# Performance work log

Measured on AMD Instinct MI355X. Metric: run time of the kernel, lower is better.

The kernel has to match this reference:

```python
import jax, jax.numpy as jnp
import numpy as np

PI = np.pi
TAU = 1.0        # self.tau
TAU_V = 10.0     # self.tau_v
TAU_CONN = 10.0  # self.tau_conn
TAU_E = 1000.0   # self.tau_e
GW = PI / 4      # gauss_width
GH = 3.0         # gauss_height
LR = 10000.0     # hebbian lr
SPIKE_NUM = 4    # keep_top_n count
NORM_FAC_HD = 1.0


def period_bound(d):
    # wrap to (-pi, pi]
    return (d + PI) % (2.0 * PI) - PI


def dist(d):
    d = period_bound(d)
    return jnp.where(d > PI, d - 2.0 * PI, d)


def setup_inputs() -> dict:
    key = jax.random.key(0)
    ks = jax.random.split(key, 8)
    P, num, L = 20000, 256, 30
    return {
        "conn_bearing": jnp.abs(jax.random.normal(ks[0], (P, num, L), jnp.float32) * 0.1),
        "r": jax.random.uniform(ks[1], (num,), jnp.float32) * 0.1,
        "u": jax.random.uniform(ks[2], (num,), jnp.float32) * 0.5,
        "v": jax.random.uniform(ks[3], (num,), jnp.float32) * 0.1,
        "r_hpc": jax.random.uniform(ks[4], (P,), jnp.float32),
        "r_bearing": jax.random.uniform(ks[5], (L,), jnp.float32),
        "pos_estimate": jnp.zeros((1,), jnp.float32),
        "angular_velocity": jnp.float32(0.3),
        "HD": jnp.float32(0.5),
        "sen2HD_stre": jnp.float32(1.0),
        "shared_t": jnp.arange(2, dtype=jnp.float32) * 0.1,  # [0, dt]
        "noise_hd": jax.random.normal(ks[6], (num,), jnp.float32) * 0.01,
        "noise_bearing": jax.random.normal(ks[7], (L,), jnp.float32) * 0.01,
        "dt": 0.1,
    }


def reference(conn_bearing, r, u, v, r_hpc, r_bearing, pos_estimate,
              angular_velocity, HD, sen2HD_stre, shared_t,
              noise_hd, noise_bearing, dt):
    # One HdOVCModel.update step with get_HD=0, noise_stre=0.0, train=2.
    P, num, L = conn_bearing.shape
    k = 0.8 / num * 20.0
    J0 = 1.0 / num * 20.0
    m = 0.84 * TAU / TAU_V
    x = jnp.linspace(-PI, PI, num + 1)[:-1]  # ring preferred directions

    # ring connectivity kernel + its FFT (precomputed in __init__)
    d0 = dist(jnp.abs(x[0] - x))
    conn = J0 * jnp.exp(-0.5 * jnp.square(d0 / GW)) / (2.0 * PI * GW ** 2)
    conn_fft = jnp.fft.fft(conn)

    # get_center(r, x) == angle(sum(exp(1j x) * r)), done in reals
    center = jnp.arctan2(jnp.sum(jnp.sin(x) * r), jnp.sum(jnp.cos(x) * r))

    # self_motion_integrate (noise_stre = 0)
    pos_e = pos_estimate + (period_bound(center - pos_estimate) / TAU_E + angular_velocity) * dt
    pos_est = period_bound(pos_e)  # [1]
    motion_input = GH * jnp.exp(-0.25 * jnp.square(dist(x - pos_est) / GW))  # [num]
    Iext = motion_input  # get_HD == 0 branch (input_HD(HD) unused)

    # bearing input via hippocampal place weighting
    r_place = r_hpc[:P]
    index = jnp.argmax(r_place)
    norm_r = jnp.where(r_place == 0, 0.0, r_place / jnp.sum(r_place))
    # fused matmul [P,num,L]@[L] then weighted sum over P
    input_bearing = jnp.einsum('pnl,l,p->n', conn_bearing, r_bearing, norm_r)

    # recurrent ring input via circular convolution (FFT)
    Irec = jnp.real(jnp.fft.ifft(jnp.fft.fft(r) * conn_fft))
    input_total = Iext + Irec + input_bearing * sen2HD_stre

    # derivative() is linear with CONSTANT coupling terms (uses self.u/self.v,
    # not the integrated state), so odeint has an exact closed form:
    # du/dt = (-u + Cu)/tau, dv/dt = (-v + Cv)/tau_v
    t = shared_t[1] - shared_t[0]
    Cu = input_total - v
    Cv = m * u
    u_sol = Cu + (u - Cu) * jnp.exp(-t / TAU)
    v_sol = Cv + (v - Cv) * jnp.exp(-t / TAU_V)
    u_new = jnp.maximum(u_sol, 0.0)
    v_new = v_sol
    r1 = jnp.square(u_new)
    r_new = r1 / (1.0 + k * jnp.sum(r1))

    # conn_update (train == 2): gather row -> top-k Hebb -> normalize -> scatter
    cb_row = conn_bearing[index]                         # [num, L]
    r_hd = r_new * (1.0 + jnp.abs(noise_hd))
    topv = jax.lax.top_k(r_hd, SPIKE_NUM)[0]
    r_learn = jnp.where(r_hd >= topv[-1], r_hd, 0.0)     # keep_top_n
    rb = r_bearing + jnp.abs(noise_bearing)
    corr = jnp.outer(r_learn, rb)                        # [num, L]
    d_b = LR * corr * cb_row / TAU_CONN * dt
    cb = cb_row + d_b
    cb = NORM_FAC_HD * cb / jnp.sum(cb, axis=1, keepdims=True)  # normalize_rows
    conn_bearing_new = conn_bearing.at[index].set(cb)

    return r_new, u_new, v_new, conn_bearing_new
```

## Files before the change

kernel.cpp:

```cpp
#include <hip/hip_runtime.h>

#define PI_F 3.14159265358979323846f
#define TWO_PI_F 6.28318530717958647692f

#define TAU_F 1.0f
#define TAU_V_F 10.0f
#define TAU_CONN_F 10.0f
#define TAU_E_F 1000.0f
#define GW_F (PI_F / 4.0f)
#define GH_F 3.0f
#define LR_F 10000.0f

#define NUMN 256
#define LB 30
#define SLAB (NUMN * LB)
#define SLAB4 (SLAB / 4)

__device__ __forceinline__ float pbf(float d) {
  float m = fmodf(d + PI_F, TWO_PI_F);
  if (m < 0.f) m += TWO_PI_F;
  return m - PI_F;
}

__global__ __launch_bounds__(256) void k_reduce_hpc(const float* __restrict__ r_hpc,
                                                    int P, float* __restrict__ ws) {
  __shared__ float ssum[256];
  __shared__ float smax[256];
  __shared__ int simax[256];
  int t = threadIdx.x;
  float s = 0.f;
  float bm = -1e30f;
  int bi = 0x7fffffff;
  for (int i = t; i < P; i += 256) {
    float v = r_hpc[i];
    s += v;
    if (v > bm) { bm = v; bi = i; }
  }
  ssum[t] = s; smax[t] = bm; simax[t] = bi;
  __syncthreads();
  for (int off = 128; off > 0; off >>= 1) {
    if (t < off) {
      ssum[t] += ssum[t + off];
      float vo = smax[t + off]; int io = simax[t + off];
      if (vo > smax[t] || (vo == smax[t] && io < simax[t])) { smax[t] = vo; simax[t] = io; }
    }
    __syncthreads();
  }
  if (t == 0) {
    ws[0] = ssum[0];
    ((int*)ws)[1] = simax[0];
  }
}

__global__ __launch_bounds__(256) void k_main(const float* __restrict__ cb,
                                              const float* __restrict__ r_hpc,
                                              const float* __restrict__ r_bearing,
                                              const float* __restrict__ ws_scal,
                                              float* __restrict__ partial,
                                              float* __restrict__ out_cb,
                                              int P, int chunk) {
  __shared__ __align__(16) float slab[SLAB];
  __shared__ float rbs[32];
  int t = threadIdx.x;
  int blk = blockIdx.x;
  if (t < LB) rbs[t] = r_bearing[t];
  float S = ws_scal[0];
  float acc = 0.f;
  int p0 = blk * chunk;
  int p1 = p0 + chunk; if (p1 > P) p1 = P;
  for (int p = p0; p < p1; ++p) {
    const float4* in4 = (const float4*)(cb + (size_t)p * SLAB);
    float4* o4 = (float4*)(out_cb + (size_t)p * SLAB);
    float4* s4 = (float4*)slab;
    for (int i = t; i < SLAB4; i += 256) {
      float4 v = in4[i];
      s4[i] = v;
      o4[i] = v;
    }
    __syncthreads();
    float rp = r_hpc[p];
    float w = (rp == 0.f) ? 0.f : rp / S;
    const float* row = slab + t * LB;
    float dot = 0.f;
#pragma unroll
    for (int l = 0; l < LB; ++l) dot += row[l] * rbs[l];
    acc += w * dot;
    __syncthreads();
  }
  partial[(size_t)blk * NUMN + t] = acc;
}

__global__ __launch_bounds__(256) void k_reduce_partial(const float* __restrict__ partial,
                                                        float* __restrict__ p2, int nb) {
  int t = threadIdx.x;
  int j = blockIdx.x;
  float s = 0.f;
  for (int b = j; b < nb; b += 64) s += partial[(size_t)b * NUMN + t];
  p2[(size_t)j * NUMN + t] = s;
}

__device__ __forceinline__ float block_reduce_sum(float val, float* red, int t) {
  red[t] = val;
  __syncthreads();
  for (int off = 128; off > 0; off >>= 1) {
    if (t < off) red[t] += red[t + off];
    __syncthreads();
  }
  float r0 = red[0];
  __syncthreads();
  return r0;
}

__global__ __launch_bounds__(256) void k_finish(
    const float* __restrict__ cb,
    const float* __restrict__ r, const float* __restrict__ u, const float* __restrict__ v,
    const float* __restrict__ noise_hd,
    const float* __restrict__ r_bearing, const float* __restrict__ noise_bearing,
    const float* __restrict__ pos_estimate, const float* __restrict__ angular_velocity,
    const float* __restrict__ sen2HD_stre, const float* __restrict__ shared_t,
    const float* __restrict__ dtp,
    const float* __restrict__ ws_scal, const float* __restrict__ p2,
    float* __restrict__ out) {
  __shared__ float red[256];
  __shared__ float rL[256], connL[256], rhdL[256];
  __shared__ float rbL[32];
  __shared__ float bc[8];
  int t = threadIdx.x;
  int index = ((const int*)ws_scal)[1];

  float ib = 0.f;
  for (int j = 0; j < 64; ++j) ib += p2[(size_t)j * NUMN + t];

  float x = -PI_F + (float)t * (TWO_PI_F / 256.f);
  float rt = r[t];
  rL[t] = rt;

  float ssin = block_reduce_sum(sinf(x) * rt, red, t);
  float scos = block_reduce_sum(cosf(x) * rt, red, t);

  if (t == 0) {
    float center = atan2f(ssin, scos);
    float pe = pos_estimate[0];
    float dtv = dtp[0];
    float pos_e = pe + (pbf(center - pe) / TAU_E_F + angular_velocity[0]) * dtv;
    bc[0] = pbf(pos_e);
  }
  __syncthreads();
  float pos_est = bc[0];

  {
    float J0 = 20.f / 256.f;
    float dmin = fminf((float)t, 256.f - (float)t) * (TWO_PI_F / 256.f);
    float q = dmin / GW_F;
    connL[t] = J0 * expf(-0.5f * q * q) / (TWO_PI_F * GW_F * GW_F);
  }
  __syncthreads();

  float Irec = 0.f;
  for (int m2 = 0; m2 < 256; ++m2) Irec += rL[m2] * connL[(t - m2) & 255];

  float dd = pbf(x - pos_est);
  float qq = dd / GW_F;
  float Iext = GH_F * expf(-0.25f * qq * qq);

  float input_total = Iext + Irec + ib * sen2HD_stre[0];
  float tstep = shared_t[1] - shared_t[0];
  float e1 = expf(-tstep / TAU_F);
  float e2 = expf(-tstep / TAU_V_F);
  float mcoef = 0.84f * TAU_F / TAU_V_F;

  float ut = u[t], vt = v[t];
  float Cu = input_total - vt;
  float Cv = mcoef * ut;
  float u_sol = Cu + (ut - Cu) * e1;
  float v_sol = Cv + (vt - Cv) * e2;
  float u_new = fmaxf(u_sol, 0.f);
  float r1 = u_new * u_new;
  float s1 = block_reduce_sum(r1, red, t);
  float kcoef = 0.8f / 256.f * 20.f;
  float r_new = r1 / (1.f + kcoef * s1);

  out[t] = r_new;
  out[256 + t] = u_new;
  out[512 + t] = v_sol;

  rhdL[t] = r_new * (1.f + fabsf(noise_hd[t]));
  if (t < LB) rbL[t] = r_bearing[t] + fabsf(noise_bearing[t]);
  __syncthreads();

  if (t == 0) {
    int e0 = -1, e1i = -1, e2i = -1, e3 = -1;
    float thr = 0.f;
    for (int pass = 0; pass < 4; ++pass) {
      float bm = -1e30f; int bi = -1;
      for (int i2 = 0; i2 < 256; ++i2) {
        if (i2 == e0 || i2 == e1i || i2 == e2i || i2 == e3) continue;
        float vv = rhdL[i2];
        if (vv > bm) { bm = vv; bi = i2; }
      }
      if (pass == 0) e0 = bi; else if (pass == 1) e1i = bi; else if (pass == 2) e2i = bi; else e3 = bi;
      thr = bm;
    }
    bc[1] = thr;
  }
  __syncthreads();
  float thr = bc[1];
  float r_learn = (rhdL[t] >= thr) ? rhdL[t] : 0.f;

  float dtv = dtp[0];
  float fac = (LR_F / TAU_CONN_F) * dtv;
  const float* rowp = cb + ((size_t)index * NUMN + t) * LB;
  float vals[LB];
  float s = 0.f;
#pragma unroll
  for (int l = 0; l < LB; ++l) {
    float vv = rowp[l] * (1.f + fac * r_learn * rbL[l]);
    vals[l] = vv;
    s += vv;
  }
  float inv = 1.f / s;
  float* orow = out + 768 + ((size_t)index * NUMN + t) * LB;
#pragma unroll
  for (int l = 0; l < LB; ++l) orow[l] = vals[l] * inv;
}

extern "C" void kernel_launch(void* const* d_in, const int* in_sizes, int n_in,
                              void* d_out, int out_size, void* d_ws, size_t ws_size,
                              hipStream_t stream) {
  const float* conn_bearing = (const float*)d_in[0];
  const float* r            = (const float*)d_in[1];
  const float* u            = (const float*)d_in[2];
  const float* v            = (const float*)d_in[3];
  const float* r_hpc        = (const float*)d_in[4];
  const float* r_bearing    = (const float*)d_in[5];
  const float* pos_estimate = (const float*)d_in[6];
  const float* angular_vel  = (const float*)d_in[7];
  const float* sen2HD       = (const float*)d_in[9];
  const float* shared_t     = (const float*)d_in[10];
  const float* noise_hd     = (const float*)d_in[11];
  const float* noise_bear   = (const float*)d_in[12];
  const float* dtp          = (const float*)d_in[13];

  int P = in_sizes[4];

  float* out = (float*)d_out;
  float* ws = (float*)d_ws;

  const int OFF_P2 = 16;
  const int OFF_PART = OFF_P2 + 64 * NUMN;

  int nb = 2000;
  {
    size_t avail = ws_size / 4;
    if (avail < (size_t)OFF_PART + NUMN) {
      nb = 1;
    } else {
      size_t maxnb = (avail - OFF_PART) / NUMN;
      if ((size_t)nb > maxnb) nb = (int)maxnb;
      if (nb < 1) nb = 1;
    }
  }
  int chunk = (P + nb - 1) / nb;

  k_reduce_hpc<<<1, 256, 0, stream>>>(r_hpc, P, ws);
  k_main<<<nb, 256, 0, stream>>>(conn_bearing, r_hpc, r_bearing, ws,
                                 ws + OFF_PART, out + 768, P, chunk);
  k_reduce_partial<<<64, 256, 0, stream>>>(ws + OFF_PART, ws + OFF_P2, nb);
  k_finish<<<1, 256, 0, stream>>>(conn_bearing, r, u, v, noise_hd, r_bearing, noise_bear,
                                  pos_estimate, angular_vel, sen2HD, shared_t, dtp,
                                  ws, ws + OFF_P2, out);
}
```

Before: 368.0 us.

## Drop LDS staging in main pass; process two slabs per iteration with nontemporal copy

Removes the shared-memory slab staging and per-slab barriers in the main streaming kernel. Each iteration now copies two slabs to the output with nontemporal stores, and each half of the block computes dot products for one slab by reading global rows directly, relying on cache hits. r_bearing is held in registers, launch bounds request 3 blocks per CU, and the block count rises from 2000 to 2500. The cost is re-reading slab data from global/cache for the dot products and higher register pressure.

```diff
diff --git a/kernel.cpp b/kernel.cpp
--- a/kernel.cpp
+++ b/kernel.cpp
@@ -15,6 +15,9 @@
 #define LB 30
 #define SLAB (NUMN * LB)
 #define SLAB4 (SLAB / 4)
+
+typedef float fx4 __attribute__((ext_vector_type(4)));
+typedef float fx2 __attribute__((ext_vector_type(2)));
 
 __device__ __forceinline__ float pbf(float d) {
   float m = fmodf(d + PI_F, TWO_PI_F);
@@ -52,42 +55,80 @@
   }
 }
 
-__global__ __launch_bounds__(256) void k_main(const float* __restrict__ cb,
-                                              const float* __restrict__ r_hpc,
-                                              const float* __restrict__ r_bearing,
-                                              const float* __restrict__ ws_scal,
-                                              float* __restrict__ partial,
-                                              float* __restrict__ out_cb,
-                                              int P, int chunk) {
-  __shared__ __align__(16) float slab[SLAB];
-  __shared__ float rbs[32];
+__global__ __launch_bounds__(256, 3) void k_main(const float* __restrict__ cb,
+                                                 const float* __restrict__ r_hpc,
+                                                 const float* __restrict__ r_bearing,
+                                                 const float* __restrict__ ws_scal,
+                                                 float* __restrict__ partial,
+                                                 float* __restrict__ out_cb,
+                                                 int P, int chunk) {
+  __shared__ float pacc[2][NUMN];
   int t = threadIdx.x;
   int blk = blockIdx.x;
-  if (t < LB) rbs[t] = r_bearing[t];
   float S = ws_scal[0];
-  float acc = 0.f;
+
+  float rbv[LB];
+#pragma unroll
+  for (int l = 0; l < LB; ++l) rbv[l] = r_bearing[l];
+
+  int which = t >> 7;
+  int pair  = t & 127;
+  int n0 = pair * 2;
+
+  float acc0 = 0.f, acc1 = 0.f, accT = 0.f;
+
   int p0 = blk * chunk;
   int p1 = p0 + chunk; if (p1 > P) p1 = P;
-  for (int p = p0; p < p1; ++p) {
-    const float4* in4 = (const float4*)(cb + (size_t)p * SLAB);
-    float4* o4 = (float4*)(out_cb + (size_t)p * SLAB);
-    float4* s4 = (float4*)slab;
+  int p = p0;
+  for (; p + 1 < p1; p += 2) {
+    const fx4* __restrict__ in4 = (const fx4*)(cb + (size_t)p * SLAB);
+    fx4* __restrict__ o4 = (fx4*)(out_cb + (size_t)p * SLAB);
+#pragma unroll
+    for (int k = 0; k < 15; ++k) {
+      int i = t + k * 256;
+      fx4 tmp = in4[i];
+      __builtin_nontemporal_store(tmp, o4 + i);
+    }
+    int pp = p + which;
+    float rp = r_hpc[pp];
+    float w = (rp == 0.f) ? 0.f : rp / S;
+    const fx4* __restrict__ row4 = (const fx4*)(cb + (size_t)pp * SLAB + n0 * LB);
+    float d0 = 0.f, d1 = 0.f;
+#pragma unroll
+    for (int k = 0; k < 15; ++k) {
+      fx4 vv = row4[k];
+      int e = 4 * k;
+      if (e + 0 < LB) d0 += vv.x * rbv[e + 0]; else d1 += vv.x * rbv[e + 0 - LB];
+      if (e + 1 < LB) d0 += vv.y * rbv[e + 1]; else d1 += vv.y * rbv[e + 1 - LB];
+      if (e + 2 < LB) d0 += vv.z * rbv[e + 2]; else d1 += vv.z * rbv[e + 2 - LB];
+      if (e + 3 < LB) d0 += vv.w * rbv[e + 3]; else d1 += vv.w * rbv[e + 3 - LB];
+    }
+    acc0 += w * d0;
+    acc1 += w * d1;
+  }
+  if (p < p1) {
+    const fx4* __restrict__ in4 = (const fx4*)(cb + (size_t)p * SLAB);
+    fx4* __restrict__ o4 = (fx4*)(out_cb + (size_t)p * SLAB);
     for (int i = t; i < SLAB4; i += 256) {
-      float4 v = in4[i];
-      s4[i] = v;
-      o4[i] = v;
-    }
-    __syncthreads();
+      fx4 tmp = in4[i];
+      __builtin_nontemporal_store(tmp, o4 + i);
+    }
     float rp = r_hpc[p];
     float w = (rp == 0.f) ? 0.f : rp / S;
-    const float* row = slab + t * LB;
-    float dot = 0.f;
-#pragma unroll
-    for (int l = 0; l < LB; ++l) dot += row[l] * rbs[l];
-    acc += w * dot;
-    __syncthreads();
-  }
-  partial[(size_t)blk * NUMN + t] = acc;
+    const fx2* __restrict__ row2 = (const fx2*)(cb + (size_t)p * SLAB + t * LB);
+    float d = 0.f;
+#pragma unroll
+    for (int k = 0; k < 15; ++k) {
+      fx2 v2 = row2[k];
+      d += v2.x * rbv[2 * k] + v2.y * rbv[2 * k + 1];
+    }
+    accT = w * d;
+  }
+
+  pacc[which][n0]     = acc0;
+  pacc[which][n0 + 1] = acc1;
+  __syncthreads();
+  partial[(size_t)blk * NUMN + t] = pacc[0][t] + pacc[1][t] + accT;
 }
 
 __global__ __launch_bounds__(256) void k_reduce_partial(const float* __restrict__ partial,
@@ -249,7 +290,7 @@
   const int OFF_P2 = 16;
   const int OFF_PART = OFF_P2 + 64 * NUMN;
 
-  int nb = 2000;
+  int nb = 2500;
   {
     size_t avail = ws_size / 4;
     if (avail < (size_t)OFF_PART + NUMN) {
```

New measurement: 361.4 us. About the same (-1.8%).

## Give each wavefront its own LDS slab region and drop block barriers in k_main

Applied to the files above, without the earlier changes.

The main streaming kernel now splits each 30 KB slab so that each of the four wavefronts copies its own quarter with eight non-temporal float4 loads and stores held in registers. That quarter holds exactly the 64 rows the wavefront reduces, so the per-iteration __syncthreads pair goes away. r_bearing is held in registers, the dot product reads float2, launch bounds ask for higher occupancy, and the block count falls from 2000 to 1250. The aim is more memory-level parallelism and less barrier stalling in a bandwidth-bound copy, at the cost of relying on wavefront-level ordering of the LDS writes and reads without an explicit barrier.

```diff
diff --git a/kernel.cpp b/kernel.cpp
--- a/kernel.cpp
+++ b/kernel.cpp
@@ -15,6 +15,10 @@
 #define LB 30
 #define SLAB (NUMN * LB)
 #define SLAB4 (SLAB / 4)
+#define WREG4 480
+
+typedef float fx4 __attribute__((ext_vector_type(4)));
+typedef float fx2 __attribute__((ext_vector_type(2)));
 
 __device__ __forceinline__ float pbf(float d) {
   float m = fmodf(d + PI_F, TWO_PI_F);
@@ -52,42 +56,70 @@
   }
 }
 
-__global__ __launch_bounds__(256) void k_main(const float* __restrict__ cb,
-                                              const float* __restrict__ r_hpc,
-                                              const float* __restrict__ r_bearing,
-                                              const float* __restrict__ ws_scal,
-                                              float* __restrict__ partial,
-                                              float* __restrict__ out_cb,
-                                              int P, int chunk) {
-  __shared__ __align__(16) float slab[SLAB];
-  __shared__ float rbs[32];
+__global__ __launch_bounds__(256, 4) void k_main(const float* __restrict__ cb,
+                                                 const float* __restrict__ r_hpc,
+                                                 const float* __restrict__ r_bearing,
+                                                 const float* __restrict__ ws_scal,
+                                                 float* __restrict__ partial,
+                                                 float* __restrict__ out_cb,
+                                                 int P, int chunk) {
+  __shared__ __align__(16) float buf[4][SLAB / 4];
   int t = threadIdx.x;
-  int blk = blockIdx.x;
-  if (t < LB) rbs[t] = r_bearing[t];
+  int w = t >> 6;
+  int lane = t & 63;
   float S = ws_scal[0];
+
+  float rbv[LB];
+#pragma unroll
+  for (int l = 0; l < LB; ++l) rbv[l] = r_bearing[l];
+
+  float* wb = buf[w];
+  fx4* wb4 = (fx4*)wb;
+  const fx2* row2 = (const fx2*)(wb + lane * LB);
+
   float acc = 0.f;
-  int p0 = blk * chunk;
+  int p0 = blockIdx.x * chunk;
   int p1 = p0 + chunk; if (p1 > P) p1 = P;
+
   for (int p = p0; p < p1; ++p) {
-    const float4* in4 = (const float4*)(cb + (size_t)p * SLAB);
-    float4* o4 = (float4*)(out_cb + (size_t)p * SLAB);
-    float4* s4 = (float4*)slab;
-    for (int i = t; i < SLAB4; i += 256) {
-      float4 v = in4[i];
-      s4[i] = v;
-      o4[i] = v;
-    }
-    __syncthreads();
+    size_t base4 = (size_t)p * SLAB4 + (size_t)w * WREG4;
+    const fx4* __restrict__ in4 = (const fx4*)cb + base4;
+    fx4* __restrict__ o4 = (fx4*)out_cb + base4;
+
+    fx4 v0 = __builtin_nontemporal_load(in4 + lane);
+    fx4 v1 = __builtin_nontemporal_load(in4 + lane + 64);
+    fx4 v2 = __builtin_nontemporal_load(in4 + lane + 128);
+    fx4 v3 = __builtin_nontemporal_load(in4 + lane + 192);
+    fx4 v4 = __builtin_nontemporal_load(in4 + lane + 256);
+    fx4 v5 = __builtin_nontemporal_load(in4 + lane + 320);
+    fx4 v6 = __builtin_nontemporal_load(in4 + lane + 384);
+    fx4 v7;
+    if (lane < 32) v7 = __builtin_nontemporal_load(in4 + lane + 448);
+
+    __builtin_nontemporal_store(v0, o4 + lane);       wb4[lane]       = v0;
+    __builtin_nontemporal_store(v1, o4 + lane + 64);  wb4[lane + 64]  = v1;
+    __builtin_nontemporal_store(v2, o4 + lane + 128); wb4[lane + 128] = v2;
+    __builtin_nontemporal_store(v3, o4 + lane + 192); wb4[lane + 192] = v3;
+    __builtin_nontemporal_store(v4, o4 + lane + 256); wb4[lane + 256] = v4;
+    __builtin_nontemporal_store(v5, o4 + lane + 320); wb4[lane + 320] = v5;
+    __builtin_nontemporal_store(v6, o4 + lane + 384); wb4[lane + 384] = v6;
+    if (lane < 32) {
+      __builtin_nontemporal_store(v7, o4 + lane + 448);
+      wb4[lane + 448] = v7;
+    }
+
     float rp = r_hpc[p];
-    float w = (rp == 0.f) ? 0.f : rp / S;
-    const float* row = slab + t * LB;
-    float dot = 0.f;
+    float d = 0.f;
 #pragma unroll
-    for (int l = 0; l < LB; ++l) dot += row[l] * rbs[l];
-    acc += w * dot;
-    __syncthreads();
-  }
-  partial[(size_t)blk * NUMN + t] = acc;
+    for (int k = 0; k < 15; ++k) {
+      fx2 u2 = row2[k];
+      d += u2.x * rbv[2 * k] + u2.y * rbv[2 * k + 1];
+    }
+    float wgt = (rp == 0.f) ? 0.f : rp / S;
+    acc += wgt * d;
+  }
+
+  partial[(size_t)blockIdx.x * NUMN + t] = acc;
 }
 
 __global__ __launch_bounds__(256) void k_reduce_partial(const float* __restrict__ partial,
@@ -249,7 +281,7 @@
   const int OFF_P2 = 16;
   const int OFF_PART = OFF_P2 + 64 * NUMN;
 
-  int nb = 2000;
+  int nb = 1250;
   {
     size_t avail = ws_size / 4;
     if (avail < (size_t)OFF_PART + NUMN) {
```

Result: faster. 315.3 us (-14.3%).

## Stream slabs through registers with nontemporal copies and per-lane accumulators

Applied to the files above, without the earlier changes.

The main kernel no longer stages each slab in shared memory with two barriers per slab. Each wave now copies its 480-float4 quarter of the slab straight from global to output using nontemporal loads and stores, and accumulates weighted values in 32 per-lane registers. The row dot products with r_bearing are formed once at the end through a shared-memory transpose. The block count is halved and launch bounds request higher occupancy, trading register pressure for fewer syncs and less LDS traffic on a bandwidth-bound copy.

```diff
diff --git a/kernel.cpp b/kernel.cpp
--- a/kernel.cpp
+++ b/kernel.cpp
@@ -15,6 +15,9 @@
 #define LB 30
 #define SLAB (NUMN * LB)
 #define SLAB4 (SLAB / 4)
+#define WREG4 480
+
+typedef float fx4 __attribute__((ext_vector_type(4)));
 
 __device__ __forceinline__ float pbf(float d) {
   float m = fmodf(d + PI_F, TWO_PI_F);
@@ -52,42 +55,84 @@
   }
 }
 
-__global__ __launch_bounds__(256) void k_main(const float* __restrict__ cb,
-                                              const float* __restrict__ r_hpc,
-                                              const float* __restrict__ r_bearing,
-                                              const float* __restrict__ ws_scal,
-                                              float* __restrict__ partial,
-                                              float* __restrict__ out_cb,
-                                              int P, int chunk) {
-  __shared__ __align__(16) float slab[SLAB];
+__global__ __launch_bounds__(256, 4) void k_main(const float* __restrict__ cb,
+                                                 const float* __restrict__ r_hpc,
+                                                 const float* __restrict__ r_bearing,
+                                                 const float* __restrict__ ws_scal,
+                                                 float* __restrict__ partial,
+                                                 float* __restrict__ out_cb,
+                                                 int P, int chunk) {
+  __shared__ float buf[4][32][64];
   __shared__ float rbs[32];
   int t = threadIdx.x;
-  int blk = blockIdx.x;
+  int w = t >> 6;
+  int lane = t & 63;
   if (t < LB) rbs[t] = r_bearing[t];
   float S = ws_scal[0];
-  float acc = 0.f;
-  int p0 = blk * chunk;
+
+  float acc[32];
+#pragma unroll
+  for (int s = 0; s < 32; ++s) acc[s] = 0.f;
+
+  int p0 = blockIdx.x * chunk;
   int p1 = p0 + chunk; if (p1 > P) p1 = P;
+
   for (int p = p0; p < p1; ++p) {
-    const float4* in4 = (const float4*)(cb + (size_t)p * SLAB);
-    float4* o4 = (float4*)(out_cb + (size_t)p * SLAB);
-    float4* s4 = (float4*)slab;
-    for (int i = t; i < SLAB4; i += 256) {
-      float4 v = in4[i];
-      s4[i] = v;
-      o4[i] = v;
+    size_t base4 = (size_t)p * SLAB4 + (size_t)w * WREG4;
+    const fx4* __restrict__ in4 = (const fx4*)cb + base4 + lane;
+    fx4* __restrict__ o4 = (fx4*)out_cb + base4 + lane;
+
+    float rp = r_hpc[p];
+    float wgt = (rp == 0.f) ? 0.f : rp / S;
+
+    fx4 v0 = __builtin_nontemporal_load(in4);
+    fx4 v1 = __builtin_nontemporal_load(in4 + 64);
+    fx4 v2 = __builtin_nontemporal_load(in4 + 128);
+    fx4 v3 = __builtin_nontemporal_load(in4 + 192);
+    fx4 v4 = __builtin_nontemporal_load(in4 + 256);
+    fx4 v5 = __builtin_nontemporal_load(in4 + 320);
+    fx4 v6 = __builtin_nontemporal_load(in4 + 384);
+    fx4 v7 = {0.f, 0.f, 0.f, 0.f};
+    if (lane < 32) v7 = __builtin_nontemporal_load(in4 + 448);
+
+    __builtin_nontemporal_store(v0, o4);
+    __builtin_nontemporal_store(v1, o4 + 64);
+    __builtin_nontemporal_store(v2, o4 + 128);
+    __builtin_nontemporal_store(v3, o4 + 192);
+    __builtin_nontemporal_store(v4, o4 + 256);
+    __builtin_nontemporal_store(v5, o4 + 320);
+    __builtin_nontemporal_store(v6, o4 + 384);
+    if (lane < 32) __builtin_nontemporal_store(v7, o4 + 448);
+
+    acc[0]  += wgt * v0.x;  acc[1]  += wgt * v0.y;  acc[2]  += wgt * v0.z;  acc[3]  += wgt * v0.w;
+    acc[4]  += wgt * v1.x;  acc[5]  += wgt * v1.y;  acc[6]  += wgt * v1.z;  acc[7]  += wgt * v1.w;
+    acc[8]  += wgt * v2.x;  acc[9]  += wgt * v2.y;  acc[10] += wgt * v2.z;  acc[11] += wgt * v2.w;
+    acc[12] += wgt * v3.x;  acc[13] += wgt * v3.y;  acc[14] += wgt * v3.z;  acc[15] += wgt * v3.w;
+    acc[16] += wgt * v4.x;  acc[17] += wgt * v4.y;  acc[18] += wgt * v4.z;  acc[19] += wgt * v4.w;
+    acc[20] += wgt * v5.x;  acc[21] += wgt * v5.y;  acc[22] += wgt * v5.z;  acc[23] += wgt * v5.w;
+    acc[24] += wgt * v6.x;  acc[25] += wgt * v6.y;  acc[26] += wgt * v6.z;  acc[27] += wgt * v6.w;
+    acc[28] += wgt * v7.x;  acc[29] += wgt * v7.y;  acc[30] += wgt * v7.z;  acc[31] += wgt * v7.w;
+  }
+
+  __syncthreads();
+#pragma unroll
+  for (int k = 0; k < 8; ++k) {
+#pragma unroll
+    for (int e = 0; e < 4; ++e) {
+      int flat = 256 * k + 4 * lane + e;
+      buf[w][4 * k + e][lane] = acc[4 * k + e] * rbs[flat % 30];
     }
-    __syncthreads();
-    float rp = r_hpc[p];
-    float w = (rp == 0.f) ? 0.f : rp / S;
-    const float* row = slab + t * LB;
-    float dot = 0.f;
-#pragma unroll
-    for (int l = 0; l < LB; ++l) dot += row[l] * rbs[l];
-    acc += w * dot;
-    __syncthreads();
-  }
-  partial[(size_t)blk * NUMN + t] = acc;
+  }
+  __syncthreads();
+
+  int r = t & 63, wv = t >> 6;
+  float s = 0.f;
+#pragma unroll
+  for (int j = 0; j < 30; ++j) {
+    int flat = 30 * r + j;
+    s += buf[wv][4 * (flat >> 8) + (flat & 3)][(flat & 255) >> 2];
+  }
+  partial[(size_t)blockIdx.x * NUMN + t] = s;
 }
 
 __global__ __launch_bounds__(256) void k_reduce_partial(const float* __restrict__ partial,
@@ -249,7 +294,7 @@
   const int OFF_P2 = 16;
   const int OFF_PART = OFF_P2 + 64 * NUMN;
 
-  int nb = 2000;
+  int nb = 1000;
   {
     size_t avail = ws_size / 4;
     if (avail < (size_t)OFF_PART + NUMN) {
```

After: 324.9 us. -11.7%, faster.
